# Kernel tuning notes

Hardware: AMD Instinct MI355X
Metric: run time of the kernel (lower is better)

Reference implementation:

```python
import jax, jax.numpy as jnp
import numpy as np

NEG = -1000000000.0

def setup_inputs() -> dict:
    key = jax.random.key(0)
    k1, k2, k3, k4 = jax.random.split(key, 4)
    B, S, D = 8, 4096, 256
    query = jax.random.normal(k1, (B, S, D), dtype=jnp.float32)
    k_ = jax.random.normal(k2, (B, S, D), dtype=jnp.float32)
    value = jax.random.normal(k3, (B, S, D), dtype=jnp.float32)
    mask = jax.random.bernoulli(k4, 0.1, (B, S, 1))  # True = masked
    return {"query": query, "key": k_, "value": value, "mask": mask}

def reference(query, key, value, mask):
    # a: [B,S,1] sum of squares of query; b: [B,S,1] for key
    a = jnp.sum(query * query, axis=-1, keepdims=True)
    b = jnp.sum(key * key, axis=-1, keepdims=True)
    # s1 = (K^T / b) @ V  -> [B, D, D]; divide each key row s by b_s
    s1 = jnp.einsum('bsd,bse->bde', key / b, value)
    # score = Q / a, masked rows set to -1e9
    score = query / a
    score = jnp.where(mask, NEG, score)
    s2 = jnp.einsum('bsd,bde->bse', score, s1)
    return s2 / query.shape[-1]
```

## Files before the change

### kernel.cpp

```cpp
#include <hip/hip_runtime.h>

#define BB 8
#define SS 4096
#define DD 256
#define NEGV -1000000000.0f

typedef float f32x4 __attribute__((ext_vector_type(4)));
typedef short s16x8 __attribute__((ext_vector_type(8)));

static __device__ __forceinline__ unsigned short f2bf(float x) {
  unsigned int u = __builtin_bit_cast(unsigned int, x);
  u += 0x7fffu + ((u >> 16) & 1u);
  return (unsigned short)(u >> 16);
}

__global__ __launch_bounds__(256) void prep_kernel(
    const float* __restrict__ Q, const float* __restrict__ K,
    const float* __restrict__ V, const int* __restrict__ mask,
    unsigned short* __restrict__ QS, unsigned short* __restrict__ KT,
    unsigned short* __restrict__ VT) {
  __shared__ unsigned short tile[DD * 34];
  const int b = blockIdx.y;
  const int s0 = blockIdx.x * 32;
  const int tid = threadIdx.x;
  const int w = tid >> 6, l = tid & 63;

  if (blockIdx.z == 0) {
#pragma unroll
    for (int it = 0; it < 8; ++it) {
      const int s = s0 + w * 8 + it;
      const size_t rowo = ((size_t)b * SS + s) * DD;
      const float4 q = *(const float4*)(Q + rowo + l * 4);
      float ss = q.x * q.x + q.y * q.y + q.z * q.z + q.w * q.w;
#pragma unroll
      for (int off = 32; off; off >>= 1) ss += __shfl_xor(ss, off);
      const int m = mask[b * SS + s];
      const float ca = m ? 0.0f : (1.0f / ss);
      const float aa = m ? NEGV : 0.0f;
      ushort4 o;
      o.x = f2bf(q.x * ca + aa);
      o.y = f2bf(q.y * ca + aa);
      o.z = f2bf(q.z * ca + aa);
      o.w = f2bf(q.w * ca + aa);
      *(ushort4*)(QS + rowo + l * 4) = o;
    }
    return;
  }

  const int isK = (blockIdx.z == 1);
  const float* __restrict__ src = isK ? K : V;
  unsigned short* __restrict__ dst = isK ? KT : VT;

#pragma unroll
  for (int it = 0; it < 8; ++it) {
    const int sl = w * 8 + it;
    const size_t rowo = ((size_t)b * SS + s0 + sl) * DD;
    const float v0 = src[rowo + l];
    const float v1 = src[rowo + l + 64];
    const float v2 = src[rowo + l + 128];
    const float v3 = src[rowo + l + 192];
    float ss = v0 * v0 + v1 * v1 + v2 * v2 + v3 * v3;
#pragma unroll
    for (int off = 32; off; off >>= 1) ss += __shfl_xor(ss, off);
    const float sc = isK ? (1.0f / ss) : 1.0f;
    tile[(l) * 34 + sl] = f2bf(v0 * sc);
    tile[(l + 64) * 34 + sl] = f2bf(v1 * sc);
    tile[(l + 128) * 34 + sl] = f2bf(v2 * sc);
    tile[(l + 192) * 34 + sl] = f2bf(v3 * sc);
  }
  __syncthreads();
  const size_t base = ((size_t)b * DD + tid) * SS + s0;
#pragma unroll
  for (int c = 0; c < 4; ++c) {
    uint4 vv;
    vv.x = *(const unsigned int*)(tile + tid * 34 + c * 8 + 0);
    vv.y = *(const unsigned int*)(tile + tid * 34 + c * 8 + 2);
    vv.z = *(const unsigned int*)(tile + tid * 34 + c * 8 + 4);
    vv.w = *(const unsigned int*)(tile + tid * 34 + c * 8 + 6);
    *(uint4*)(dst + base + c * 8) = vv;
  }
}

__global__ __launch_bounds__(256) void p2_kernel(
    const unsigned short* __restrict__ KT, const unsigned short* __restrict__ VT,
    float* __restrict__ part, int nks) {
  __shared__ unsigned short vt_l[128 * 40];
  __shared__ unsigned short kt_l[128 * 40];
  const int b = blockIdx.z;
  const int d0 = (blockIdx.x & 1) * 128;
  const int e0 = (blockIdx.x >> 1) * 128;
  const int sbeg = blockIdx.y * nks * 32;
  const int tid = threadIdx.x;
  const int w = tid >> 6, l = tid & 63;
  const int wr = w & 1, wc = w >> 1;
  const int quad = l >> 4, mr = l & 15;

  f32x4 acc[4][4];
#pragma unroll
  for (int i = 0; i < 4; ++i)
#pragma unroll
    for (int j = 0; j < 4; ++j) acc[i][j] = (f32x4){0.f, 0.f, 0.f, 0.f};

  const size_t vbase = ((size_t)b * DD + e0) * SS;
  const size_t kbase = ((size_t)b * DD + d0) * SS;

  for (int ks = 0; ks < nks; ++ks) {
    const int sc = sbeg + ks * 32;
#pragma unroll
    for (int it = 0; it < 2; ++it) {
      const int flat = it * 256 + tid;
      const int row = flat >> 2;
      const int c8 = (flat & 3) * 8;
      *(uint4*)(vt_l + row * 40 + c8) =
          *(const uint4*)(VT + vbase + (size_t)row * SS + sc + c8);
      *(uint4*)(kt_l + row * 40 + c8) =
          *(const uint4*)(KT + kbase + (size_t)row * SS + sc + c8);
    }
    __syncthreads();
    s16x8 af[4], bfr[4];
#pragma unroll
    for (int i = 0; i < 4; ++i)
      af[i] = *(const s16x8*)(vt_l + (wr * 64 + i * 16 + mr) * 40 + quad * 8);
#pragma unroll
    for (int j = 0; j < 4; ++j)
      bfr[j] = *(const s16x8*)(kt_l + (wc * 64 + j * 16 + mr) * 40 + quad * 8);
#pragma unroll
    for (int i = 0; i < 4; ++i)
#pragma unroll
      for (int j = 0; j < 4; ++j)
        acc[i][j] = __builtin_amdgcn_mfma_f32_16x16x32_bf16(af[i], bfr[j],
                                                            acc[i][j], 0, 0, 0);
    __syncthreads();
  }

  float* pb = part + (((size_t)blockIdx.y * BB + b) * DD) * DD;
#pragma unroll
  for (int i = 0; i < 4; ++i) {
    const int e = e0 + wr * 64 + i * 16 + quad * 4;
#pragma unroll
    for (int j = 0; j < 4; ++j) {
      const int d = d0 + wc * 64 + j * 16 + mr;
      float* p = pb + (size_t)e * DD + d;
#pragma unroll
      for (int r = 0; r < 4; ++r) p[(size_t)r * DD] = acc[i][j][r];
    }
  }
}

__global__ __launch_bounds__(256) void reduce_kernel(
    const float* __restrict__ part, unsigned short* __restrict__ s1b,
    int split) {
  const size_t i4 = ((size_t)blockIdx.x * 256 + threadIdx.x) * 4;
  float ax = 0.f, ay = 0.f, az = 0.f, aw = 0.f;
  for (int p = 0; p < split; ++p) {
    const float4 v = *(const float4*)(part + (size_t)p * (BB * DD * DD) + i4);
    ax += v.x; ay += v.y; az += v.z; aw += v.w;
  }
  ushort4 o;
  o.x = f2bf(ax); o.y = f2bf(ay); o.z = f2bf(az); o.w = f2bf(aw);
  *(ushort4*)(s1b + i4) = o;
}

__global__ __launch_bounds__(256) void p3_kernel(
    const unsigned short* __restrict__ QS, const unsigned short* __restrict__ s1b,
    float* __restrict__ out) {
  __shared__ unsigned short qs_l[128 * 40];
  __shared__ unsigned short s1_l[128 * 40];
  const int b = blockIdx.z;
  const int e0 = blockIdx.x * 128;
  const int s0 = blockIdx.y * 128;
  const int tid = threadIdx.x;
  const int w = tid >> 6, l = tid & 63;
  const int wr = w & 1, wc = w >> 1;
  const int quad = l >> 4, mr = l & 15;

  f32x4 acc[4][4];
#pragma unroll
  for (int i = 0; i < 4; ++i)
#pragma unroll
    for (int j = 0; j < 4; ++j) acc[i][j] = (f32x4){0.f, 0.f, 0.f, 0.f};

  for (int ks = 0; ks < 8; ++ks) {
    const int dc = ks * 32;
#pragma unroll
    for (int it = 0; it < 2; ++it) {
      const int flat = it * 256 + tid;
      const int row = flat >> 2;
      const int c8 = (flat & 3) * 8;
      *(uint4*)(qs_l + row * 40 + c8) =
          *(const uint4*)(QS + ((size_t)b * SS + s0 + row) * DD + dc + c8);
      *(uint4*)(s1_l + row * 40 + c8) =
          *(const uint4*)(s1b + ((size_t)b * DD + e0 + row) * DD + dc + c8);
    }
    __syncthreads();
    s16x8 af[4], bfr[4];
#pragma unroll
    for (int i = 0; i < 4; ++i)
      af[i] = *(const s16x8*)(qs_l + (wr * 64 + i * 16 + mr) * 40 + quad * 8);
#pragma unroll
    for (int j = 0; j < 4; ++j)
      bfr[j] = *(const s16x8*)(s1_l + (wc * 64 + j * 16 + mr) * 40 + quad * 8);
#pragma unroll
    for (int i = 0; i < 4; ++i)
#pragma unroll
      for (int j = 0; j < 4; ++j)
        acc[i][j] = __builtin_amdgcn_mfma_f32_16x16x32_bf16(af[i], bfr[j],
                                                            acc[i][j], 0, 0, 0);
    __syncthreads();
  }

#pragma unroll
  for (int i = 0; i < 4; ++i) {
    const int s = s0 + wr * 64 + i * 16 + quad * 4;
#pragma unroll
    for (int j = 0; j < 4; ++j) {
      const int e = e0 + wc * 64 + j * 16 + mr;
      float* p = out + ((size_t)b * SS + s) * DD + e;
#pragma unroll
      for (int r = 0; r < 4; ++r) p[(size_t)r * DD] = acc[i][j][r] * (1.0f / DD);
    }
  }
}

extern "C" void kernel_launch(void* const* d_in, const int* in_sizes, int n_in,
                              void* d_out, int out_size, void* d_ws,
                              size_t ws_size, hipStream_t stream) {
  const float* Q = (const float*)d_in[0];
  const float* K = (const float*)d_in[1];
  const float* V = (const float*)d_in[2];
  const int* mask = (const int*)d_in[3];
  float* out = (float*)d_out;

  char* ws = (char*)d_ws;
  const size_t MB = (size_t)1024 * 1024;
  unsigned short* QS = (unsigned short*)(ws);
  unsigned short* KT = (unsigned short*)(ws + 16 * MB);
  unsigned short* VT = (unsigned short*)(ws + 32 * MB);
  float* part = (float*)(ws + 48 * MB);

  const int split = (ws_size >= (size_t)84 * MB) ? 16 : 8;
  const int nks = SS / (32 * split);
  unsigned short* s1b =
      (unsigned short*)(ws + 48 * MB + (size_t)split * 2 * MB);

  prep_kernel<<<dim3(SS / 32, BB, 3), 256, 0, stream>>>(Q, K, V, mask, QS, KT,
                                                        VT);
  p2_kernel<<<dim3(4, split, BB), 256, 0, stream>>>(KT, VT, part, nks);
  reduce_kernel<<<dim3(512), 256, 0, stream>>>(part, s1b, split);
  p3_kernel<<<dim3(2, SS / 128, BB), 256, 0, stream>>>(QS, s1b, out);
}
```

Measured before the change: 185.3 us.

## Use direct global-to-LDS loads with 64-wide K tiles and restructure prep transpose

Both GEMM kernels now load their tiles with the global_load_lds builtin straight into unpadded 64-wide LDS tiles. This halves the number of K iterations and barriers and removes the register round-trip on loads. The prep kernel processes 64 rows per block with float4 loads batched in registers and interleaved shuffle reductions, then transposes through a wider LDS tile. The unpadded 64-element row stride may cause LDS bank conflicts on fragment reads, and the prep transpose now reads scalar shorts from LDS.

```diff
diff --git a/kernel.cpp b/kernel.cpp
--- a/kernel.cpp
+++ b/kernel.cpp
@@ -12,6 +12,13 @@
   unsigned int u = __builtin_bit_cast(unsigned int, x);
   u += 0x7fffu + ((u >> 16) & 1u);
   return (unsigned short)(u >> 16);
+}
+
+static __device__ __forceinline__ void gload_lds16(
+    const unsigned short* __restrict__ g, unsigned short* l) {
+  __builtin_amdgcn_global_load_lds(
+      (const __attribute__((address_space(1))) void*)g,
+      (__attribute__((address_space(3))) void*)l, 16, 0, 0);
 }
 
 __global__ __launch_bounds__(256) void prep_kernel(
@@ -19,30 +26,38 @@
     const float* __restrict__ V, const int* __restrict__ mask,
     unsigned short* __restrict__ QS, unsigned short* __restrict__ KT,
     unsigned short* __restrict__ VT) {
-  __shared__ unsigned short tile[DD * 34];
+  __shared__ unsigned short tile[64 * 260];
   const int b = blockIdx.y;
-  const int s0 = blockIdx.x * 32;
+  const int s0 = blockIdx.x * 64;
   const int tid = threadIdx.x;
   const int w = tid >> 6, l = tid & 63;
 
   if (blockIdx.z == 0) {
-#pragma unroll
-    for (int it = 0; it < 8; ++it) {
-      const int s = s0 + w * 8 + it;
-      const size_t rowo = ((size_t)b * SS + s) * DD;
-      const float4 q = *(const float4*)(Q + rowo + l * 4);
-      float ss = q.x * q.x + q.y * q.y + q.z * q.z + q.w * q.w;
-#pragma unroll
-      for (int off = 32; off; off >>= 1) ss += __shfl_xor(ss, off);
-      const int m = mask[b * SS + s];
-      const float ca = m ? 0.0f : (1.0f / ss);
+    float4 reg[16];
+    float ps[16];
+#pragma unroll
+    for (int it = 0; it < 16; ++it) {
+      const int row = it * 4 + w;
+      reg[it] = *(const float4*)(Q + ((size_t)b * SS + s0 + row) * DD + l * 4);
+      ps[it] = reg[it].x * reg[it].x + reg[it].y * reg[it].y +
+               reg[it].z * reg[it].z + reg[it].w * reg[it].w;
+    }
+#pragma unroll
+    for (int off = 32; off; off >>= 1)
+#pragma unroll
+      for (int it = 0; it < 16; ++it) ps[it] += __shfl_xor(ps[it], off);
+#pragma unroll
+    for (int it = 0; it < 16; ++it) {
+      const int row = it * 4 + w;
+      const int m = mask[b * SS + s0 + row];
+      const float ca = m ? 0.0f : (1.0f / ps[it]);
       const float aa = m ? NEGV : 0.0f;
       ushort4 o;
-      o.x = f2bf(q.x * ca + aa);
-      o.y = f2bf(q.y * ca + aa);
-      o.z = f2bf(q.z * ca + aa);
-      o.w = f2bf(q.w * ca + aa);
-      *(ushort4*)(QS + rowo + l * 4) = o;
+      o.x = f2bf(reg[it].x * ca + aa);
+      o.y = f2bf(reg[it].y * ca + aa);
+      o.z = f2bf(reg[it].z * ca + aa);
+      o.w = f2bf(reg[it].w * ca + aa);
+      *(ushort4*)(QS + ((size_t)b * SS + s0 + row) * DD + l * 4) = o;
     }
     return;
   }
@@ -51,49 +66,63 @@
   const float* __restrict__ src = isK ? K : V;
   unsigned short* __restrict__ dst = isK ? KT : VT;
 
-#pragma unroll
-  for (int it = 0; it < 8; ++it) {
-    const int sl = w * 8 + it;
-    const size_t rowo = ((size_t)b * SS + s0 + sl) * DD;
-    const float v0 = src[rowo + l];
-    const float v1 = src[rowo + l + 64];
-    const float v2 = src[rowo + l + 128];
-    const float v3 = src[rowo + l + 192];
-    float ss = v0 * v0 + v1 * v1 + v2 * v2 + v3 * v3;
-#pragma unroll
-    for (int off = 32; off; off >>= 1) ss += __shfl_xor(ss, off);
-    const float sc = isK ? (1.0f / ss) : 1.0f;
-    tile[(l) * 34 + sl] = f2bf(v0 * sc);
-    tile[(l + 64) * 34 + sl] = f2bf(v1 * sc);
-    tile[(l + 128) * 34 + sl] = f2bf(v2 * sc);
-    tile[(l + 192) * 34 + sl] = f2bf(v3 * sc);
+  float4 reg[16];
+  float ps[16];
+#pragma unroll
+  for (int it = 0; it < 16; ++it) {
+    const int row = it * 4 + w;
+    reg[it] = *(const float4*)(src + ((size_t)b * SS + s0 + row) * DD + l * 4);
+    ps[it] = reg[it].x * reg[it].x + reg[it].y * reg[it].y +
+             reg[it].z * reg[it].z + reg[it].w * reg[it].w;
+  }
+  float scl[16];
+  if (isK) {
+#pragma unroll
+    for (int off = 32; off; off >>= 1)
+#pragma unroll
+      for (int it = 0; it < 16; ++it) ps[it] += __shfl_xor(ps[it], off);
+#pragma unroll
+    for (int it = 0; it < 16; ++it) scl[it] = 1.0f / ps[it];
+  } else {
+#pragma unroll
+    for (int it = 0; it < 16; ++it) scl[it] = 1.0f;
+  }
+#pragma unroll
+  for (int it = 0; it < 16; ++it) {
+    const int row = it * 4 + w;
+    ushort4 o;
+    o.x = f2bf(reg[it].x * scl[it]);
+    o.y = f2bf(reg[it].y * scl[it]);
+    o.z = f2bf(reg[it].z * scl[it]);
+    o.w = f2bf(reg[it].w * scl[it]);
+    *(ushort4*)(tile + row * 260 + l * 4) = o;
   }
   __syncthreads();
-  const size_t base = ((size_t)b * DD + tid) * SS + s0;
-#pragma unroll
-  for (int c = 0; c < 4; ++c) {
-    uint4 vv;
-    vv.x = *(const unsigned int*)(tile + tid * 34 + c * 8 + 0);
-    vv.y = *(const unsigned int*)(tile + tid * 34 + c * 8 + 2);
-    vv.z = *(const unsigned int*)(tile + tid * 34 + c * 8 + 4);
-    vv.w = *(const unsigned int*)(tile + tid * 34 + c * 8 + 6);
-    *(uint4*)(dst + base + c * 8) = vv;
+  const size_t gbase = ((size_t)b * DD + tid) * SS + s0;
+#pragma unroll
+  for (int c = 0; c < 8; ++c) {
+    union { unsigned short h[8]; uint4 v; } u;
+#pragma unroll
+    for (int j = 0; j < 8; ++j) u.h[j] = tile[(c * 8 + j) * 260 + tid];
+    *(uint4*)(dst + gbase + c * 8) = u.v;
   }
 }
 
 __global__ __launch_bounds__(256) void p2_kernel(
     const unsigned short* __restrict__ KT, const unsigned short* __restrict__ VT,
-    float* __restrict__ part, int nks) {
-  __shared__ unsigned short vt_l[128 * 40];
-  __shared__ unsigned short kt_l[128 * 40];
+    float* __restrict__ part, int iters) {
+  __shared__ unsigned short vt_l[128 * 64];
+  __shared__ unsigned short kt_l[128 * 64];
   const int b = blockIdx.z;
   const int d0 = (blockIdx.x & 1) * 128;
   const int e0 = (blockIdx.x >> 1) * 128;
-  const int sbeg = blockIdx.y * nks * 32;
+  const int sbeg = blockIdx.y * iters * 64;
   const int tid = threadIdx.x;
   const int w = tid >> 6, l = tid & 63;
   const int wr = w & 1, wc = w >> 1;
   const int quad = l >> 4, mr = l & 15;
+  const int lr = l >> 3;
+  const int lc = (l & 7) * 8;
 
   f32x4 acc[4][4];
 #pragma unroll
@@ -104,36 +133,35 @@
   const size_t vbase = ((size_t)b * DD + e0) * SS;
   const size_t kbase = ((size_t)b * DD + d0) * SS;
 
-  for (int ks = 0; ks < nks; ++ks) {
-    const int sc = sbeg + ks * 32;
-#pragma unroll
-    for (int it = 0; it < 2; ++it) {
-      const int flat = it * 256 + tid;
-      const int row = flat >> 2;
-      const int c8 = (flat & 3) * 8;
-      *(uint4*)(vt_l + row * 40 + c8) =
-          *(const uint4*)(VT + vbase + (size_t)row * SS + sc + c8);
-      *(uint4*)(kt_l + row * 40 + c8) =
-          *(const uint4*)(KT + kbase + (size_t)row * SS + sc + c8);
-    }
-    __syncthreads();
-    s16x8 af[4], bfr[4];
-#pragma unroll
-    for (int i = 0; i < 4; ++i)
-      af[i] = *(const s16x8*)(vt_l + (wr * 64 + i * 16 + mr) * 40 + quad * 8);
-#pragma unroll
-    for (int j = 0; j < 4; ++j)
-      bfr[j] = *(const s16x8*)(kt_l + (wc * 64 + j * 16 + mr) * 40 + quad * 8);
-#pragma unroll
-    for (int i = 0; i < 4; ++i)
+  for (int ks = 0; ks < iters; ++ks) {
+    const int sc = sbeg + ks * 64;
+#pragma unroll
+    for (int c = 0; c < 4; ++c) {
+      const int r0 = w * 32 + c * 8;
+      gload_lds16(VT + vbase + (size_t)(r0 + lr) * SS + sc + lc, vt_l + r0 * 64);
+      gload_lds16(KT + kbase + (size_t)(r0 + lr) * SS + sc + lc, kt_l + r0 * 64);
+    }
+    __syncthreads();
+#pragma unroll
+    for (int kh = 0; kh < 2; ++kh) {
+      s16x8 af[4], bfr[4];
+#pragma unroll
+      for (int i = 0; i < 4; ++i)
+        af[i] = *(const s16x8*)(vt_l + (wr * 64 + i * 16 + mr) * 64 + kh * 32 + quad * 8);
 #pragma unroll
       for (int j = 0; j < 4; ++j)
-        acc[i][j] = __builtin_amdgcn_mfma_f32_16x16x32_bf16(af[i], bfr[j],
-                                                            acc[i][j], 0, 0, 0);
-    __syncthreads();
-  }
-
-  float* pb = part + (((size_t)blockIdx.y * BB + b) * DD) * DD;
+        bfr[j] = *(const s16x8*)(kt_l + (wc * 64 + j * 16 + mr) * 64 + kh * 32 + quad * 8);
+#pragma unroll
+      for (int i = 0; i < 4; ++i)
+#pragma unroll
+        for (int j = 0; j < 4; ++j)
+          acc[i][j] = __builtin_amdgcn_mfma_f32_16x16x32_bf16(af[i], bfr[j],
+                                                              acc[i][j], 0, 0, 0);
+    }
+    __syncthreads();
+  }
+
+  float* pb = part + ((size_t)blockIdx.y * BB + b) * DD * DD;
 #pragma unroll
   for (int i = 0; i < 4; ++i) {
     const int e = e0 + wr * 64 + i * 16 + quad * 4;
@@ -164,8 +192,8 @@
 __global__ __launch_bounds__(256) void p3_kernel(
     const unsigned short* __restrict__ QS, const unsigned short* __restrict__ s1b,
     float* __restrict__ out) {
-  __shared__ unsigned short qs_l[128 * 40];
-  __shared__ unsigned short s1_l[128 * 40];
+  __shared__ unsigned short qs_l[128 * 64];
+  __shared__ unsigned short s1_l[128 * 64];
   const int b = blockIdx.z;
   const int e0 = blockIdx.x * 128;
   const int s0 = blockIdx.y * 128;
@@ -173,6 +201,8 @@
   const int w = tid >> 6, l = tid & 63;
   const int wr = w & 1, wc = w >> 1;
   const int quad = l >> 4, mr = l & 15;
+  const int lr = l >> 3;
+  const int lc = (l & 7) * 8;
 
   f32x4 acc[4][4];
 #pragma unroll
@@ -180,32 +210,33 @@
 #pragma unroll
     for (int j = 0; j < 4; ++j) acc[i][j] = (f32x4){0.f, 0.f, 0.f, 0.f};
 
-  for (int ks = 0; ks < 8; ++ks) {
-    const int dc = ks * 32;
-#pragma unroll
-    for (int it = 0; it < 2; ++it) {
-      const int flat = it * 256 + tid;
-      const int row = flat >> 2;
-      const int c8 = (flat & 3) * 8;
-      *(uint4*)(qs_l + row * 40 + c8) =
-          *(const uint4*)(QS + ((size_t)b * SS + s0 + row) * DD + dc + c8);
-      *(uint4*)(s1_l + row * 40 + c8) =
-          *(const uint4*)(s1b + ((size_t)b * DD + e0 + row) * DD + dc + c8);
-    }
-    __syncthreads();
-    s16x8 af[4], bfr[4];
-#pragma unroll
-    for (int i = 0; i < 4; ++i)
-      af[i] = *(const s16x8*)(qs_l + (wr * 64 + i * 16 + mr) * 40 + quad * 8);
-#pragma unroll
-    for (int j = 0; j < 4; ++j)
-      bfr[j] = *(const s16x8*)(s1_l + (wc * 64 + j * 16 + mr) * 40 + quad * 8);
-#pragma unroll
-    for (int i = 0; i < 4; ++i)
+  for (int ks = 0; ks < 4; ++ks) {
+    const int dc = ks * 64;
+#pragma unroll
+    for (int c = 0; c < 4; ++c) {
+      const int r0 = w * 32 + c * 8;
+      gload_lds16(QS + ((size_t)b * SS + s0 + r0 + lr) * DD + dc + lc,
+                  qs_l + r0 * 64);
+      gload_lds16(s1b + ((size_t)b * DD + e0 + r0 + lr) * DD + dc + lc,
+                  s1_l + r0 * 64);
+    }
+    __syncthreads();
+#pragma unroll
+    for (int kh = 0; kh < 2; ++kh) {
+      s16x8 af[4], bfr[4];
+#pragma unroll
+      for (int i = 0; i < 4; ++i)
+        af[i] = *(const s16x8*)(qs_l + (wr * 64 + i * 16 + mr) * 64 + kh * 32 + quad * 8);
 #pragma unroll
       for (int j = 0; j < 4; ++j)
-        acc[i][j] = __builtin_amdgcn_mfma_f32_16x16x32_bf16(af[i], bfr[j],
-                                                            acc[i][j], 0, 0, 0);
+        bfr[j] = *(const s16x8*)(s1_l + (wc * 64 + j * 16 + mr) * 64 + kh * 32 + quad * 8);
+#pragma unroll
+      for (int i = 0; i < 4; ++i)
+#pragma unroll
+        for (int j = 0; j < 4; ++j)
+          acc[i][j] = __builtin_amdgcn_mfma_f32_16x16x32_bf16(af[i], bfr[j],
+                                                              acc[i][j], 0, 0, 0);
+    }
     __syncthreads();
   }
 
@@ -238,14 +269,14 @@
   unsigned short* VT = (unsigned short*)(ws + 32 * MB);
   float* part = (float*)(ws + 48 * MB);
 
-  const int split = (ws_size >= (size_t)84 * MB) ? 16 : 8;
-  const int nks = SS / (32 * split);
+  const int split = (ws_size >= (size_t)82 * MB) ? 16 : 8;
+  const int iters = SS / (64 * split);
   unsigned short* s1b =
       (unsigned short*)(ws + 48 * MB + (size_t)split * 2 * MB);
 
-  prep_kernel<<<dim3(SS / 32, BB, 3), 256, 0, stream>>>(Q, K, V, mask, QS, KT,
+  prep_kernel<<<dim3(SS / 64, BB, 3), 256, 0, stream>>>(Q, K, V, mask, QS, KT,
                                                         VT);
-  p2_kernel<<<dim3(4, split, BB), 256, 0, stream>>>(KT, VT, part, nks);
+  p2_kernel<<<dim3(4, split, BB), 256, 0, stream>>>(KT, VT, part, iters);
   reduce_kernel<<<dim3(512), 256, 0, stream>>>(part, s1b, split);
   p3_kernel<<<dim3(2, SS / 128, BB), 256, 0, stream>>>(QS, s1b, out);
 }
```

Result: faster. 180.1 us (-2.8%).
